# Kernel optimization log

Hardware: AMD Instinct MI355X
Metric: run time of the kernel (lower is better)

The kernel has to match this reference:

```python
import jax, jax.numpy as jnp
import numpy as np

N_SCALES = 3
BASE_SIGMA = 0.1
SCALES = jnp.asarray([BASE_SIGMA * 2.0 ** i for i in range(N_SCALES)], dtype=jnp.float32)


def setup_inputs() -> dict:
    key = jax.random.key(0)
    k_x, k_pos, k_tp, k_w1, k_b1, k_w2, k_b2 = jax.random.split(key, 7)
    B, C, T = 16, 306, 4000
    M = 128
    x = jax.random.normal(k_x, (B, C, T), dtype=jnp.float32)
    positions = jax.random.normal(k_pos, (B, C, 2), dtype=jnp.float32)
    target_positions = jax.random.normal(k_tp, (M, 2), dtype=jnp.float32)
    # nn.Linear(3, 32) / nn.Linear(32, 1) params (kaiming-uniform-ish init)
    lim1 = 1.0 / np.sqrt(3.0)
    w1 = jax.random.uniform(k_w1, (3, 32), jnp.float32, -lim1, lim1)
    b1 = jax.random.uniform(k_b1, (32,), jnp.float32, -lim1, lim1)
    lim2 = 1.0 / np.sqrt(32.0)
    w2 = jax.random.uniform(k_w2, (32, 1), jnp.float32, -lim2, lim2)
    b2 = jax.random.uniform(k_b2, (1,), jnp.float32, -lim2, lim2)
    return {"x": x, "positions": positions, "target_positions": target_positions,
            "w1": w1, "b1": b1, "w2": w2, "b2": b2}


def reference(x, positions, target_positions, w1, b1, w2, b2):
    # squared euclidean distances [B, C, M]
    diff = positions[:, :, None, :] - target_positions[None, None, :, :]
    d2 = jnp.sum(diff * diff, axis=-1)
    # multi-scale Gaussian kernels, stacked on last axis -> [B, C, M, n_scales]
    inv = 1.0 / (2.0 * SCALES ** 2)  # [n_scales]
    scale_weights = jnp.exp(-d2[..., None] * inv)
    # tiny 2-layer MLP gate: (3 -> 32 -> 1)
    h = jax.nn.relu(scale_weights @ w1 + b1)  # [B, C, M, 32]
    w = (h @ w2 + b2)[..., 0]                 # [B, C, M]
    # normalize over channel dim
    w = w / (jnp.sum(w, axis=1, keepdims=True) + 1e-8)
    # weighted channel aggregation -> [B, M, T]
    return jnp.einsum('bct,bcm->bmt', x, w)
```

## Files before the change

kernel.cpp:

```cpp
#include <hip/hip_runtime.h>

#define B_ 16
#define C_ 306
#define T_ 4000
#define M_ 128

typedef short bf16x8 __attribute__((ext_vector_type(8)));
typedef float f32x4 __attribute__((ext_vector_type(4)));

#define WF_PER_B 81920

__global__ __launch_bounds__(320)
void gate_kernel(const float* __restrict__ positions,
                 const float* __restrict__ target,
                 const float* __restrict__ w1,
                 const float* __restrict__ b1,
                 const float* __restrict__ w2,
                 const float* __restrict__ b2,
                 unsigned short* __restrict__ wf,
                 float* __restrict__ scale) {
    const int b  = blockIdx.x >> 5;
    const int mg = blockIdx.x & 31;
    const int tid = threadIdx.x;

    __shared__ float s_w1[96], s_b1[32], s_w2[32];
    __shared__ float s_b2;
    __shared__ float s_tgt[8];
    __shared__ float s_part[4][5];
    __shared__ unsigned short s_frag[40 * 72];

    if (tid < 96) s_w1[tid] = w1[tid];
    if (tid < 32) { s_b1[tid] = b1[tid]; s_w2[tid] = w2[tid]; }
    if (tid == 256) s_b2 = b2[0];
    if (tid >= 312) s_tgt[tid - 312] = target[mg * 8 + (tid - 312)];
    __syncthreads();

    float px = 0.0f, py = 0.0f;
    if (tid < C_) {
        px = positions[(b * C_ + tid) * 2 + 0];
        py = positions[(b * C_ + tid) * 2 + 1];
    }

    float wv_[4];
#pragma unroll
    for (int mi = 0; mi < 4; ++mi) {
        float w = 0.0f;
        if (tid < C_) {
            const float dx = px - s_tgt[mi * 2 + 0];
            const float dy = py - s_tgt[mi * 2 + 1];
            const float d2 = dx * dx + dy * dy;
            const float s2 = __expf(-d2 * 3.125f);
            const float q  = s2 * s2;
            const float s1 = q * q;
            const float r  = s1 * s1;
            const float s0 = r * r;
            float acc = s_b2;
#pragma unroll
            for (int j = 0; j < 32; ++j) {
                float h = fmaf(s0, s_w1[j],
                          fmaf(s1, s_w1[32 + j],
                          fmaf(s2, s_w1[64 + j], s_b1[j])));
                acc = fmaf(fmaxf(h, 0.0f), s_w2[j], acc);
            }
            w = acc;
        }
        wv_[mi] = w;
    }

#pragma unroll
    for (int mi = 0; mi < 4; ++mi) {
        float s = wv_[mi];
#pragma unroll
        for (int off = 32; off > 0; off >>= 1) s += __shfl_down(s, off, 64);
        if ((tid & 63) == 0) s_part[mi][tid >> 6] = s;
    }

    const int chunk = tid >> 3;
    const int slot  = tid & 7;
#pragma unroll
    for (int mi = 0; mi < 4; ++mi) {
        const float w = wv_[mi];
        const unsigned int u = __float_as_uint(w);
        const unsigned short h = (unsigned short)(u >> 16);
        const float lof = w - __uint_as_float(u & 0xffff0000u);
        const unsigned short l = (unsigned short)(__float_as_uint(lof) >> 16);
        s_frag[chunk * 72 + mi * 16 + 0 + slot] = h;
        s_frag[chunk * 72 + mi * 16 + 8 + slot] = l;
    }
    __syncthreads();

    if (tid < 4) {
        float tot = s_part[tid][0] + s_part[tid][1] + s_part[tid][2]
                  + s_part[tid][3] + s_part[tid][4];
        scale[b * M_ + mg * 4 + tid] = 1.0f / (tot + 1e-8f);
    }

    {
        const int ch = tid >> 3;
        const int g  = tid & 7;
        const uint4 v = *(const uint4*)(s_frag + ch * 72 + g * 8);
        unsigned short* dst = wf + (size_t)b * WF_PER_B
                            + (size_t)ch * 2048 + mg * 64 + g * 8;
        *(uint4*)dst = v;
    }
}

#define RUNSTRIDE 648

__global__ __launch_bounds__(256, 2)
void merge_gemm(const float* __restrict__ x,
                const unsigned short* __restrict__ wf,
                const float* __restrict__ scale,
                float* __restrict__ out) {
    const int t0 = blockIdx.x * 128;
    const int b  = blockIdx.y;
    const int tid  = threadIdx.x;
    const int lane = tid & 63;
    const int wv   = tid >> 6;
    const int tquad = lane >> 4;
    const int tsub  = lane & 15;

    __shared__ __align__(16) unsigned int sXh[2][4 * RUNSTRIDE];
    __shared__ __align__(16) unsigned int sXl[2][4 * RUNSTRIDE];
    __shared__ __align__(16) float sScale[M_];

    if (tid < M_) sScale[tid] = scale[b * M_ + tid];

    const float* xb = x + (size_t)b * C_ * T_;
    const unsigned short* wfB = wf + (size_t)b * WF_PER_B;

    f32x4 acc[4][4];
#pragma unroll
    for (int i = 0; i < 4; ++i)
#pragma unroll
        for (int j = 0; j < 4; ++j) acc[i][j] = (f32x4){0.f, 0.f, 0.f, 0.f};

    const int mw = (wv & 1) * 64;
    const int tw = (wv >> 1) * 64;

    const int cpB = tid >> 5;
    const int TQ  = tid & 31;
    const float* xcol = xb + min(t0 + TQ * 4, T_ - 4);

    auto loadX = [&](int k, float4* xv) {
#pragma unroll
        for (int sub = 0; sub < 2; ++sub) {
            const int cp = cpB + 8 * sub;
            const int c  = k * 32 + 2 * cp;
            xv[sub * 2 + 0] = *(const float4*)(xcol + (size_t)min(c,     C_ - 1) * T_);
            xv[sub * 2 + 1] = *(const float4*)(xcol + (size_t)min(c + 1, C_ - 1) * T_);
        }
    };
    auto loadW = [&](int k, bf16x8* ah_, bf16x8* al_) {
#pragma unroll
        for (int mi = 0; mi < 4; ++mi) {
            const size_t aoff = ((size_t)(k * 4 + tquad) * 128
                               + (mw + mi * 16 + tsub)) * 16;
            ah_[mi] = *(const bf16x8*)(wfB + aoff);
            al_[mi] = *(const bf16x8*)(wfB + aoff + 8);
        }
    };
    auto packX = [&](const float4* xv, unsigned int* Dh, unsigned int* Dl) {
#pragma unroll
        for (int sub = 0; sub < 2; ++sub) {
            const int cp  = cpB + 8 * sub;
            const int run = cp >> 2;
            const int pw  = cp & 3;
            const float* fa = (const float*)&xv[sub * 2 + 0];
            const float* fb = (const float*)&xv[sub * 2 + 1];
            const int base = run * RUNSTRIDE + TQ * 20 + pw;
#pragma unroll
            for (int tt = 0; tt < 4; ++tt) {
                const unsigned int ua = __float_as_uint(fa[tt]);
                const unsigned int ub = __float_as_uint(fb[tt]);
                const float la = fa[tt] - __uint_as_float(ua & 0xffff0000u);
                const float lb = fb[tt] - __uint_as_float(ub & 0xffff0000u);
                Dh[base + tt * 4] = __builtin_amdgcn_perm(ub, ua, 0x07060302u);
                Dl[base + tt * 4] = __builtin_amdgcn_perm(__float_as_uint(lb),
                                                          __float_as_uint(la),
                                                          0x07060302u);
            }
        }
    };

    bf16x8 ah[4], al[4];
    float4 xv0[4], xv1[4];
    loadX(0, xv0);
    loadX(1, xv1);
    loadW(0, ah, al);
    packX(xv0, &sXh[0][0], &sXl[0][0]);
    asm volatile("s_waitcnt lgkmcnt(0)" ::: "memory");
    __builtin_amdgcn_s_barrier();
    asm volatile("" ::: "memory");

    auto step = [&](const int k, float4 (&xnext)[4], float4 (&xfetch)[4]) {
        if (k < 8) loadX(k + 2, xfetch);

        const unsigned int* Sh = &sXh[k & 1][0];
        const unsigned int* Sl = &sXl[k & 1][0];
        bf16x8 bh[4], bl[4];
#pragma unroll
        for (int i = 0; i < 4; ++i) {
            const int t = tw + i * 16 + tsub;
            const int a = tquad * RUNSTRIDE + (t >> 2) * 20 + (t & 3) * 4;
            bh[i] = *(const bf16x8*)(Sh + a);
            bl[i] = *(const bf16x8*)(Sl + a);
        }

#pragma unroll
        for (int mi = 0; mi < 4; ++mi)
#pragma unroll
            for (int ti = 0; ti < 4; ++ti)
                acc[mi][ti] = __builtin_amdgcn_mfma_f32_16x16x32_bf16(
                    ah[mi], bh[ti], acc[mi][ti], 0, 0, 0);
#pragma unroll
        for (int mi = 0; mi < 4; ++mi)
#pragma unroll
            for (int ti = 0; ti < 4; ++ti)
                acc[mi][ti] = __builtin_amdgcn_mfma_f32_16x16x32_bf16(
                    ah[mi], bl[ti], acc[mi][ti], 0, 0, 0);
#pragma unroll
        for (int mi = 0; mi < 4; ++mi)
#pragma unroll
            for (int ti = 0; ti < 4; ++ti)
                acc[mi][ti] = __builtin_amdgcn_mfma_f32_16x16x32_bf16(
                    al[mi], bh[ti], acc[mi][ti], 0, 0, 0);

        if (k < 9) {
            loadW(k + 1, ah, al);
            packX(xnext, &sXh[(k + 1) & 1][0], &sXl[(k + 1) & 1][0]);
            asm volatile("s_waitcnt lgkmcnt(0)" ::: "memory");
            __builtin_amdgcn_s_barrier();
            asm volatile("" ::: "memory");
        }
    };

#pragma unroll
    for (int kk = 0; kk < 5; ++kk) {
        step(2 * kk,     xv1, xv0);
        step(2 * kk + 1, xv0, xv1);
    }

#pragma unroll
    for (int mi = 0; mi < 4; ++mi) {
        const int mbase = mw + mi * 16 + tquad * 4;
        const float4 sc = *(const float4*)(sScale + mbase);
        float* op = out + ((size_t)b * M_ + mbase) * T_;
#pragma unroll
        for (int ti = 0; ti < 4; ++ti) {
            const int tg = t0 + tw + ti * 16 + tsub;
            if (tg < T_) {
                op[(size_t)0 * T_ + tg] = acc[mi][ti][0] * sc.x;
                op[(size_t)1 * T_ + tg] = acc[mi][ti][1] * sc.y;
                op[(size_t)2 * T_ + tg] = acc[mi][ti][2] * sc.z;
                op[(size_t)3 * T_ + tg] = acc[mi][ti][3] * sc.w;
            }
        }
    }
}

extern "C" void kernel_launch(void* const* d_in, const int* in_sizes, int n_in,
                              void* d_out, int out_size, void* d_ws, size_t ws_size,
                              hipStream_t stream) {
    const float* x         = (const float*)d_in[0];
    const float* positions = (const float*)d_in[1];
    const float* target    = (const float*)d_in[2];
    const float* w1        = (const float*)d_in[3];
    const float* b1        = (const float*)d_in[4];
    const float* b2_dummy  = (const float*)d_in[6];
    const float* w2        = (const float*)d_in[5];
    const float* b2        = b2_dummy;
    float* out = (float*)d_out;

    float* scale = (float*)d_ws;
    unsigned short* wf = (unsigned short*)(scale + B_ * M_);

    gate_kernel<<<B_ * 32, 320, 0, stream>>>(positions, target, w1, b1, w2, b2,
                                             wf, scale);

    dim3 grid((T_ + 127) / 128, B_);
    merge_gemm<<<grid, 256, 0, stream>>>(x, wf, scale, out);
}
```

Baseline: 144.9 us.

## Halve merge GEMM time tile to 64 and raise occupancy to four blocks

Shrinks the merge GEMM's time tile from 128 to 64 columns per block, which doubles the grid and halves the accumulator registers. Launch bounds now allow four blocks per CU. The x prefetch is reduced from two steps ahead to one to free registers. The aim is better latency hiding through more parallelism on a bandwidth-bound kernel, at the cost of reloading the weight fragments twice as often and a shallower prefetch.

```diff
diff --git a/kernel.cpp b/kernel.cpp
--- a/kernel.cpp
+++ b/kernel.cpp
@@ -105,14 +105,14 @@
     }
 }
 
-#define RUNSTRIDE 648
-
-__global__ __launch_bounds__(256, 2)
+#define RS2 328
+
+__global__ __launch_bounds__(256, 4)
 void merge_gemm(const float* __restrict__ x,
                 const unsigned short* __restrict__ wf,
                 const float* __restrict__ scale,
                 float* __restrict__ out) {
-    const int t0 = blockIdx.x * 128;
+    const int t0 = blockIdx.x * 64;
     const int b  = blockIdx.y;
     const int tid  = threadIdx.x;
     const int lane = tid & 63;
@@ -120,8 +120,8 @@
     const int tquad = lane >> 4;
     const int tsub  = lane & 15;
 
-    __shared__ __align__(16) unsigned int sXh[2][4 * RUNSTRIDE];
-    __shared__ __align__(16) unsigned int sXl[2][4 * RUNSTRIDE];
+    __shared__ __align__(16) unsigned int sXh[2][4 * RS2];
+    __shared__ __align__(16) unsigned int sXl[2][4 * RS2];
     __shared__ __align__(16) float sScale[M_];
 
     if (tid < M_) sScale[tid] = scale[b * M_ + tid];
@@ -129,27 +129,23 @@
     const float* xb = x + (size_t)b * C_ * T_;
     const unsigned short* wfB = wf + (size_t)b * WF_PER_B;
 
-    f32x4 acc[4][4];
+    f32x4 acc[4][2];
 #pragma unroll
     for (int i = 0; i < 4; ++i)
 #pragma unroll
-        for (int j = 0; j < 4; ++j) acc[i][j] = (f32x4){0.f, 0.f, 0.f, 0.f};
-
-    const int mw = (wv & 1) * 64;
-    const int tw = (wv >> 1) * 64;
-
-    const int cpB = tid >> 5;
-    const int TQ  = tid & 31;
+        for (int j = 0; j < 2; ++j) acc[i][j] = (f32x4){0.f, 0.f, 0.f, 0.f};
+
+    const int mw  = (wv & 1) * 64;
+    const int tw2 = (wv >> 1) * 32;
+
+    const int cp = tid >> 4;
+    const int TQ = tid & 15;
     const float* xcol = xb + min(t0 + TQ * 4, T_ - 4);
 
     auto loadX = [&](int k, float4* xv) {
-#pragma unroll
-        for (int sub = 0; sub < 2; ++sub) {
-            const int cp = cpB + 8 * sub;
-            const int c  = k * 32 + 2 * cp;
-            xv[sub * 2 + 0] = *(const float4*)(xcol + (size_t)min(c,     C_ - 1) * T_);
-            xv[sub * 2 + 1] = *(const float4*)(xcol + (size_t)min(c + 1, C_ - 1) * T_);
-        }
+        const int c = k * 32 + 2 * cp;
+        xv[0] = *(const float4*)(xcol + (size_t)min(c,     C_ - 1) * T_);
+        xv[1] = *(const float4*)(xcol + (size_t)min(c + 1, C_ - 1) * T_);
     };
     auto loadW = [&](int k, bf16x8* ah_, bf16x8* al_) {
 #pragma unroll
@@ -161,48 +157,47 @@
         }
     };
     auto packX = [&](const float4* xv, unsigned int* Dh, unsigned int* Dl) {
-#pragma unroll
-        for (int sub = 0; sub < 2; ++sub) {
-            const int cp  = cpB + 8 * sub;
-            const int run = cp >> 2;
-            const int pw  = cp & 3;
-            const float* fa = (const float*)&xv[sub * 2 + 0];
-            const float* fb = (const float*)&xv[sub * 2 + 1];
-            const int base = run * RUNSTRIDE + TQ * 20 + pw;
-#pragma unroll
-            for (int tt = 0; tt < 4; ++tt) {
-                const unsigned int ua = __float_as_uint(fa[tt]);
-                const unsigned int ub = __float_as_uint(fb[tt]);
-                const float la = fa[tt] - __uint_as_float(ua & 0xffff0000u);
-                const float lb = fb[tt] - __uint_as_float(ub & 0xffff0000u);
-                Dh[base + tt * 4] = __builtin_amdgcn_perm(ub, ua, 0x07060302u);
-                Dl[base + tt * 4] = __builtin_amdgcn_perm(__float_as_uint(lb),
-                                                          __float_as_uint(la),
-                                                          0x07060302u);
-            }
+        const int run = cp >> 2;
+        const int pw  = cp & 3;
+        const float* fa = (const float*)&xv[0];
+        const float* fb = (const float*)&xv[1];
+        const int base = run * RS2 + TQ * 20 + pw;
+#pragma unroll
+        for (int tt = 0; tt < 4; ++tt) {
+            const unsigned int ua = __float_as_uint(fa[tt]);
+            const unsigned int ub = __float_as_uint(fb[tt]);
+            const float la = fa[tt] - __uint_as_float(ua & 0xffff0000u);
+            const float lb = fb[tt] - __uint_as_float(ub & 0xffff0000u);
+            Dh[base + tt * 4] = __builtin_amdgcn_perm(ub, ua, 0x07060302u);
+            Dl[base + tt * 4] = __builtin_amdgcn_perm(__float_as_uint(lb),
+                                                      __float_as_uint(la),
+                                                      0x07060302u);
         }
     };
 
     bf16x8 ah[4], al[4];
-    float4 xv0[4], xv1[4];
-    loadX(0, xv0);
-    loadX(1, xv1);
-    loadW(0, ah, al);
-    packX(xv0, &sXh[0][0], &sXl[0][0]);
+    {
+        float4 xv[2];
+        loadX(0, xv);
+        loadW(0, ah, al);
+        packX(xv, &sXh[0][0], &sXl[0][0]);
+    }
     asm volatile("s_waitcnt lgkmcnt(0)" ::: "memory");
     __builtin_amdgcn_s_barrier();
     asm volatile("" ::: "memory");
 
-    auto step = [&](const int k, float4 (&xnext)[4], float4 (&xfetch)[4]) {
-        if (k < 8) loadX(k + 2, xfetch);
+#pragma unroll
+    for (int k = 0; k < 10; ++k) {
+        float4 xn[2];
+        if (k < 9) loadX(k + 1, xn);
 
         const unsigned int* Sh = &sXh[k & 1][0];
         const unsigned int* Sl = &sXl[k & 1][0];
-        bf16x8 bh[4], bl[4];
-#pragma unroll
-        for (int i = 0; i < 4; ++i) {
-            const int t = tw + i * 16 + tsub;
-            const int a = tquad * RUNSTRIDE + (t >> 2) * 20 + (t & 3) * 4;
+        bf16x8 bh[2], bl[2];
+#pragma unroll
+        for (int i = 0; i < 2; ++i) {
+            const int t = tw2 + i * 16 + tsub;
+            const int a = tquad * RS2 + (t >> 2) * 20 + (t & 3) * 4;
             bh[i] = *(const bf16x8*)(Sh + a);
             bl[i] = *(const bf16x8*)(Sl + a);
         }
@@ -210,35 +205,29 @@
 #pragma unroll
         for (int mi = 0; mi < 4; ++mi)
 #pragma unroll
-            for (int ti = 0; ti < 4; ++ti)
+            for (int ti = 0; ti < 2; ++ti)
                 acc[mi][ti] = __builtin_amdgcn_mfma_f32_16x16x32_bf16(
                     ah[mi], bh[ti], acc[mi][ti], 0, 0, 0);
 #pragma unroll
         for (int mi = 0; mi < 4; ++mi)
 #pragma unroll
-            for (int ti = 0; ti < 4; ++ti)
+            for (int ti = 0; ti < 2; ++ti)
                 acc[mi][ti] = __builtin_amdgcn_mfma_f32_16x16x32_bf16(
                     ah[mi], bl[ti], acc[mi][ti], 0, 0, 0);
 #pragma unroll
         for (int mi = 0; mi < 4; ++mi)
 #pragma unroll
-            for (int ti = 0; ti < 4; ++ti)
+            for (int ti = 0; ti < 2; ++ti)
                 acc[mi][ti] = __builtin_amdgcn_mfma_f32_16x16x32_bf16(
                     al[mi], bh[ti], acc[mi][ti], 0, 0, 0);
 
         if (k < 9) {
             loadW(k + 1, ah, al);
-            packX(xnext, &sXh[(k + 1) & 1][0], &sXl[(k + 1) & 1][0]);
+            packX(xn, &sXh[(k + 1) & 1][0], &sXl[(k + 1) & 1][0]);
             asm volatile("s_waitcnt lgkmcnt(0)" ::: "memory");
             __builtin_amdgcn_s_barrier();
             asm volatile("" ::: "memory");
         }
-    };
-
-#pragma unroll
-    for (int kk = 0; kk < 5; ++kk) {
-        step(2 * kk,     xv1, xv0);
-        step(2 * kk + 1, xv0, xv1);
     }
 
 #pragma unroll
@@ -247,8 +236,8 @@
         const float4 sc = *(const float4*)(sScale + mbase);
         float* op = out + ((size_t)b * M_ + mbase) * T_;
 #pragma unroll
-        for (int ti = 0; ti < 4; ++ti) {
-            const int tg = t0 + tw + ti * 16 + tsub;
+        for (int ti = 0; ti < 2; ++ti) {
+            const int tg = t0 + tw2 + ti * 16 + tsub;
             if (tg < T_) {
                 op[(size_t)0 * T_ + tg] = acc[mi][ti][0] * sc.x;
                 op[(size_t)1 * T_ + tg] = acc[mi][ti][1] * sc.y;
@@ -267,9 +256,8 @@
     const float* target    = (const float*)d_in[2];
     const float* w1        = (const float*)d_in[3];
     const float* b1        = (const float*)d_in[4];
-    const float* b2_dummy  = (const float*)d_in[6];
     const float* w2        = (const float*)d_in[5];
-    const float* b2        = b2_dummy;
+    const float* b2        = (const float*)d_in[6];
     float* out = (float*)d_out;
 
     float* scale = (float*)d_ws;
@@ -278,6 +266,6 @@
     gate_kernel<<<B_ * 32, 320, 0, stream>>>(positions, target, w1, b1, w2, b2,
                                              wf, scale);
 
-    dim3 grid((T_ + 127) / 128, B_);
+    dim3 grid((T_ + 63) / 64, B_);
     merge_gemm<<<grid, 256, 0, stream>>>(x, wf, scale, out);
 }
```

Result: slower. 154.9 us (+6.9%).
